# Performance work log

Measured on AMD Instinct MI355X. Metric: run time of the kernel, lower is better.

## Reference

```python
import jax, jax.numpy as jnp
import numpy as np

N, E, D_IN, D_HID, D_OUT = 50000, 600000, 128, 128, 64


def setup_inputs() -> dict:
    key = jax.random.key(0)
    ks = jax.random.split(key, 8)
    x = jax.random.normal(ks[0], (N, D_IN), dtype=jnp.float32)
    edge_index = jax.random.randint(ks[1], (2, E), 0, N, dtype=jnp.int64)
    def glorot(k, fan_in, fan_out):
        s = (6.0 / (fan_in + fan_out)) ** 0.5
        return jax.random.uniform(k, (fan_in, fan_out), jnp.float32, -s, s)
    return {
        "x": x,
        "W1": glorot(ks[2], D_IN, D_HID), "b1": jnp.zeros((D_HID,), jnp.float32),
        "W2": glorot(ks[3], D_HID, D_HID), "b2": jnp.zeros((D_HID,), jnp.float32),
        "W3": glorot(ks[4], D_HID, D_OUT), "b3": jnp.zeros((D_OUT,), jnp.float32),
        "edge_index": edge_index,
    }


def reference(x, W1, b1, W2, b2, W3, b3, edge_index):
    n = x.shape[0]
    # GCN with self-loops: A_hat = A + I, norm = D^-1/2 A_hat D^-1/2
    loops = jnp.arange(n, dtype=edge_index.dtype)
    row = jnp.concatenate([edge_index[0], loops])  # source nodes
    col = jnp.concatenate([edge_index[1], loops])  # target nodes
    deg = jax.ops.segment_sum(jnp.ones_like(col, dtype=x.dtype), col, num_segments=n)
    dinv = jnp.where(deg > 0, jax.lax.rsqrt(deg), 0.0)
    norm = dinv[row] * dinv[col]  # [E+N]

    def gcn_conv(h, W, b):
        hw = h @ W                                   # [N, out]
        msg = hw[row] * norm[:, None]                # [E+N, out] gather + scale
        return jax.ops.segment_sum(msg, col, num_segments=n) + b

    h = jax.nn.relu(gcn_conv(x, W1, b1))
    h = jax.nn.relu(gcn_conv(h, W2, b2))
    return gcn_conv(h, W3, b3)
```

## Files before the change

### kernel.cpp

```cpp
#include <hip/hip_runtime.h>
#include <hip/hip_bf16.h>
#include <hip/hip_fp16.h>


typedef _Float16 h2 __attribute__((ext_vector_type(2)));
typedef _Float16 h8 __attribute__((ext_vector_type(8)));

__device__ inline float4 h4_to_f4(float2 raw) {
    __half2 lo = *reinterpret_cast<__half2*>(&raw.x);
    __half2 hi = *reinterpret_cast<__half2*>(&raw.y);
    float2 a = __half22float2(lo);
    float2 b = __half22float2(hi);
    return make_float4(a.x, a.y, b.x, b.y);
}

__device__ inline uint pack_h2(float a, float b) {
    __half2 h = __floats2half2_rn(a, b);
    return *reinterpret_cast<uint*>(&h);
}

__global__ __launch_bounds__(256) void zero_counts_kernel(int4* __restrict__ p, int n4) {
    int i = blockIdx.x * 256 + threadIdx.x;
    if (i < n4) p[i] = make_int4(0, 0, 0, 0);
}

__global__ __launch_bounds__(256) void f32_to_f16_kernel(const float4* __restrict__ in,
                                                         uint2* __restrict__ out, int n4) {
    int i = blockIdx.x * 256 + threadIdx.x;
    if (i < n4) {
        float4 v = in[i];
        out[i] = make_uint2(pack_h2(v.x, v.y), pack_h2(v.z, v.w));
    }
}

__global__ void count_edges_kernel(const int* __restrict__ col, int* __restrict__ counts, int E) {
    int e = blockIdx.x * blockDim.x + threadIdx.x;
    if (e < E) atomicAdd(&counts[col[e]], 1);
}

__global__ __launch_bounds__(256) void block_sum_kernel(const int* __restrict__ counts,
                                                        int* __restrict__ blocksum, int n) {
    int i = blockIdx.x * 256 + threadIdx.x;
    int v = (i < n) ? counts[i] : 0;
    #pragma unroll
    for (int d = 1; d < 64; d <<= 1) v += __shfl_xor(v, d);
    __shared__ int ws[4];
    if ((threadIdx.x & 63) == 0) ws[threadIdx.x >> 6] = v;
    __syncthreads();
    if (threadIdx.x == 0) blocksum[blockIdx.x] = ws[0] + ws[1] + ws[2] + ws[3];
}

__global__ __launch_bounds__(256) void scan_sums_kernel(const int* __restrict__ blocksum,
                                                        int* __restrict__ blockoff,
                                                        int* __restrict__ offsets, int nb, int n) {
    int tid = threadIdx.x;
    int lane = tid & 63, wid = tid >> 6;
    int orig = (tid < nb) ? blocksum[tid] : 0;
    int v = orig;
    #pragma unroll
    for (int d = 1; d < 64; d <<= 1) {
        int u = __shfl_up(v, d);
        if (lane >= d) v += u;
    }
    __shared__ int ws[4];
    if (lane == 63) ws[wid] = v;
    __syncthreads();
    int add = 0;
    for (int w = 0; w < wid; ++w) add += ws[w];
    v += add;
    if (tid < nb) blockoff[tid] = v - orig;
    if (tid == 255) offsets[n] = v;
}

__global__ __launch_bounds__(256) void write_offsets_kernel(const int* __restrict__ counts,
                                                            const int* __restrict__ blockoff,
                                                            int* __restrict__ offsets,
                                                            int* __restrict__ cursor,
                                                            float* __restrict__ dinv, int n) {
    int tid = threadIdx.x;
    int i = blockIdx.x * 256 + tid;
    int lane = tid & 63, wid = tid >> 6;
    int c = (i < n) ? counts[i] : 0;
    int v = c;
    #pragma unroll
    for (int d = 1; d < 64; d <<= 1) {
        int u = __shfl_up(v, d);
        if (lane >= d) v += u;
    }
    __shared__ int ws[4];
    if (lane == 63) ws[wid] = v;
    __syncthreads();
    int add = 0;
    for (int w = 0; w < wid; ++w) add += ws[w];
    int incl = v + add;
    if (i < n) {
        offsets[i] = blockoff[blockIdx.x] + incl - c;
        cursor[i] = 0;
        dinv[i] = rsqrtf((float)(c + 1));
    }
}

__global__ void fill_csr_kernel(const int* __restrict__ row, const int* __restrict__ col,
                                const int* __restrict__ offsets, int* __restrict__ cursor,
                                const float* __restrict__ dinv,
                                int2* __restrict__ edges, int E) {
    int e = blockIdx.x * blockDim.x + threadIdx.x;
    if (e < E) {
        int c = col[e];
        int r = row[e];
        int pos = offsets[c] + atomicAdd(&cursor[c], 1);
        edges[pos] = make_int2(r, __float_as_int(dinv[r] * dinv[c]));
    }
}

template <int DO>
__global__ __launch_bounds__(256, 2) void gemm16_kernel(const __half* __restrict__ A,
                                                        const float* __restrict__ W,
                                                        __half* __restrict__ out, int n) {
    constexpr int K = 128;
    constexpr int COLTH = DO / 8;
    constexpr int ROWTH = 256 / COLTH;
    constexpr int R = (DO == 128) ? 8 : 4;
    constexpr int BR = ROWTH * R;
    constexpr int HALF = DO / 2;

    __shared__ alignas(16) h2 Wl[(K / 2) * DO];

    int tid = threadIdx.x;
    for (int idx = tid; idx < (K / 2) * (DO / 4); idx += 256) {
        int k2 = idx / (DO / 4);
        int c4 = idx % (DO / 4);
        float4 w0 = ((const float4*)(W + (size_t)(2 * k2) * DO))[c4];
        float4 w1 = ((const float4*)(W + (size_t)(2 * k2 + 1) * DO))[c4];
        h2* dst = &Wl[k2 * DO + c4 * 4];
        h2 d0; d0.x = (_Float16)w0.x; d0.y = (_Float16)w1.x; dst[0] = d0;
        h2 d1; d1.x = (_Float16)w0.y; d1.y = (_Float16)w1.y; dst[1] = d1;
        h2 d2; d2.x = (_Float16)w0.z; d2.y = (_Float16)w1.z; dst[2] = d2;
        h2 d3; d3.x = (_Float16)w0.w; d3.y = (_Float16)w1.w; dst[3] = d3;
    }
    __syncthreads();

    int ct = tid % COLTH;
    int rt = tid / COLTH;
    int rb = blockIdx.x * BR + rt * R;

    int rowc[R];
    #pragma unroll
    for (int i = 0; i < R; ++i) {
        int row = rb + i;
        rowc[i] = (row < n) ? row : (n - 1);
    }

    float acc[R][8];
    #pragma unroll
    for (int i = 0; i < R; ++i)
        #pragma unroll
        for (int c = 0; c < 8; ++c) acc[i][c] = 0.f;

    #pragma unroll 2
    for (int k8 = 0; k8 < K / 8; ++k8) {
        h8 av[R];
        #pragma unroll
        for (int i = 0; i < R; ++i) {
            av[i] = ((const h8*)(A + (size_t)rowc[i] * K))[k8];
        }
        #pragma unroll
        for (int kk = 0; kk < 4; ++kk) {
            int k2 = k8 * 4 + kk;
            h2 w0[4], w1[4];
            *(uint4*)w0 = *(const uint4*)(&Wl[k2 * DO + ct * 4]);
            *(uint4*)w1 = *(const uint4*)(&Wl[k2 * DO + HALF + ct * 4]);
            #pragma unroll
            for (int i = 0; i < R; ++i) {
                h2 a; a.x = av[i][2 * kk]; a.y = av[i][2 * kk + 1];
                #pragma unroll
                for (int c = 0; c < 4; ++c) {
                    acc[i][c]     = __builtin_amdgcn_fdot2(a, w0[c], acc[i][c], false);
                    acc[i][4 + c] = __builtin_amdgcn_fdot2(a, w1[c], acc[i][4 + c], false);
                }
            }
        }
    }

    #pragma unroll
    for (int i = 0; i < R; ++i) {
        int row = rb + i;
        if (row < n) {
            uint2 q0 = make_uint2(pack_h2(acc[i][0], acc[i][1]), pack_h2(acc[i][2], acc[i][3]));
            uint2 q1 = make_uint2(pack_h2(acc[i][4], acc[i][5]), pack_h2(acc[i][6], acc[i][7]));
            *(uint2*)(out + (size_t)row * DO + ct * 4) = q0;
            *(uint2*)(out + (size_t)row * DO + HALF + ct * 4) = q1;
        }
    }
}

template <int DO, bool RELU, bool F16OUT>
__global__ __launch_bounds__(256) void agg_kernel(const __half* __restrict__ hw,
                                                  const int* __restrict__ offsets,
                                                  const int2* __restrict__ edges,
                                                  const float* __restrict__ dinv,
                                                  const float* __restrict__ bias,
                                                  void* __restrict__ outp, int n) {
    constexpr int TPD = DO / 4;
    constexpr int DPB = 256 / TPD;
    int d = blockIdx.x * DPB + threadIdx.x / TPD;
    int j = threadIdx.x % TPD;
    if (d >= n) return;

    const float2* hw2 = (const float2*)hw;
    int beg = offsets[d];
    int end = offsets[d + 1];
    float di = dinv[d];
    float sw = di * di;

    float4 b4 = ((const float4*)bias)[j];
    float4 self = h4_to_f4(hw2[(size_t)d * TPD + j]);
    float4 acc;
    acc.x = b4.x + self.x * sw;
    acc.y = b4.y + self.y * sw;
    acc.z = b4.z + self.z * sw;
    acc.w = b4.w + self.w * sw;

    int e = beg;
    for (; e + 8 <= end; e += 8) {
        int2 r0 = edges[e + 0], r1 = edges[e + 1], r2 = edges[e + 2], r3 = edges[e + 3];
        int2 r4 = edges[e + 4], r5 = edges[e + 5], r6 = edges[e + 6], r7 = edges[e + 7];
        float4 v0 = h4_to_f4(hw2[(size_t)r0.x * TPD + j]);
        float4 v1 = h4_to_f4(hw2[(size_t)r1.x * TPD + j]);
        float4 v2 = h4_to_f4(hw2[(size_t)r2.x * TPD + j]);
        float4 v3 = h4_to_f4(hw2[(size_t)r3.x * TPD + j]);
        float4 v4 = h4_to_f4(hw2[(size_t)r4.x * TPD + j]);
        float4 v5 = h4_to_f4(hw2[(size_t)r5.x * TPD + j]);
        float4 v6 = h4_to_f4(hw2[(size_t)r6.x * TPD + j]);
        float4 v7 = h4_to_f4(hw2[(size_t)r7.x * TPD + j]);
        float w0 = __int_as_float(r0.y), w1 = __int_as_float(r1.y);
        float w2 = __int_as_float(r2.y), w3 = __int_as_float(r3.y);
        float w4 = __int_as_float(r4.y), w5 = __int_as_float(r5.y);
        float w6 = __int_as_float(r6.y), w7 = __int_as_float(r7.y);
        acc.x += v0.x * w0; acc.y += v0.y * w0; acc.z += v0.z * w0; acc.w += v0.w * w0;
        acc.x += v1.x * w1; acc.y += v1.y * w1; acc.z += v1.z * w1; acc.w += v1.w * w1;
        acc.x += v2.x * w2; acc.y += v2.y * w2; acc.z += v2.z * w2; acc.w += v2.w * w2;
        acc.x += v3.x * w3; acc.y += v3.y * w3; acc.z += v3.z * w3; acc.w += v3.w * w3;
        acc.x += v4.x * w4; acc.y += v4.y * w4; acc.z += v4.z * w4; acc.w += v4.w * w4;
        acc.x += v5.x * w5; acc.y += v5.y * w5; acc.z += v5.z * w5; acc.w += v5.w * w5;
        acc.x += v6.x * w6; acc.y += v6.y * w6; acc.z += v6.z * w6; acc.w += v6.w * w6;
        acc.x += v7.x * w7; acc.y += v7.y * w7; acc.z += v7.z * w7; acc.w += v7.w * w7;
    }
    for (; e + 4 <= end; e += 4) {
        int2 r0 = edges[e + 0], r1 = edges[e + 1], r2 = edges[e + 2], r3 = edges[e + 3];
        float4 v0 = h4_to_f4(hw2[(size_t)r0.x * TPD + j]);
        float4 v1 = h4_to_f4(hw2[(size_t)r1.x * TPD + j]);
        float4 v2 = h4_to_f4(hw2[(size_t)r2.x * TPD + j]);
        float4 v3 = h4_to_f4(hw2[(size_t)r3.x * TPD + j]);
        float w0 = __int_as_float(r0.y), w1 = __int_as_float(r1.y);
        float w2 = __int_as_float(r2.y), w3 = __int_as_float(r3.y);
        acc.x += v0.x * w0; acc.y += v0.y * w0; acc.z += v0.z * w0; acc.w += v0.w * w0;
        acc.x += v1.x * w1; acc.y += v1.y * w1; acc.z += v1.z * w1; acc.w += v1.w * w1;
        acc.x += v2.x * w2; acc.y += v2.y * w2; acc.z += v2.z * w2; acc.w += v2.w * w2;
        acc.x += v3.x * w3; acc.y += v3.y * w3; acc.z += v3.z * w3; acc.w += v3.w * w3;
    }
    for (; e < end; ++e) {
        int2 er = edges[e];
        float w = __int_as_float(er.y);
        float4 v = h4_to_f4(hw2[(size_t)er.x * TPD + j]);
        acc.x += v.x * w; acc.y += v.y * w; acc.z += v.z * w; acc.w += v.w * w;
    }

    if (RELU) {
        acc.x = fmaxf(acc.x, 0.f); acc.y = fmaxf(acc.y, 0.f);
        acc.z = fmaxf(acc.z, 0.f); acc.w = fmaxf(acc.w, 0.f);
    }
    if (F16OUT) {
        uint2 q = make_uint2(pack_h2(acc.x, acc.y), pack_h2(acc.z, acc.w));
        ((uint2*)outp)[(size_t)d * TPD + j] = q;
    } else {
        ((float4*)outp)[(size_t)d * TPD + j] = acc;
    }
}

extern "C" void kernel_launch(void* const* d_in, const int* in_sizes, int n_in,
                              void* d_out, int out_size, void* d_ws, size_t ws_size,
                              hipStream_t stream) {
    const float* x  = (const float*)d_in[0];
    const float* W1 = (const float*)d_in[1];
    const float* b1 = (const float*)d_in[2];
    const float* W2 = (const float*)d_in[3];
    const float* b2 = (const float*)d_in[4];
    const float* W3 = (const float*)d_in[5];
    const float* b3 = (const float*)d_in[6];
    const int*   ei = (const int*)d_in[7];

    const int N = in_sizes[0] / 128;
    const int E = in_sizes[7] / 2;
    const int* rowi = ei;
    const int* coli = ei + E;

    float* out = (float*)d_out;

    char* ws = (char*)d_ws;
    size_t off = 0;
    auto alloc = [&](size_t bytes) -> void* {
        void* p = ws + off;
        off = (off + bytes + 255) & ~(size_t)255;
        return p;
    };
    const int NB = (N + 255) / 256;
    float* dinv     = (float*)alloc((size_t)N * 4);
    int*   counts   = (int*)  alloc(((size_t)N + 4) * 4);
    int*   offsets  = (int*)  alloc((size_t)(N + 1) * 4);
    int*   cursor   = (int*)  alloc((size_t)N * 4);
    int*   blocksum = (int*)  alloc((size_t)NB * 4);
    int*   blockoff = (int*)  alloc((size_t)NB * 4);
    int2*  edges    = (int2*) alloc((size_t)E * 8);
    __half* x16     = (__half*)alloc((size_t)N * 128 * 2);
    __half* hw16    = (__half*)alloc((size_t)N * 128 * 2);
    __half* h16     = (__half*)alloc((size_t)N * 128 * 2);

    const int n4 = (N + 3) / 4;
    zero_counts_kernel<<<(n4 + 255) / 256, 256, 0, stream>>>((int4*)counts, n4);
    count_edges_kernel<<<(E + 255) / 256, 256, 0, stream>>>(coli, counts, E);
    block_sum_kernel<<<NB, 256, 0, stream>>>(counts, blocksum, N);
    scan_sums_kernel<<<1, 256, 0, stream>>>(blocksum, blockoff, offsets, NB, N);
    write_offsets_kernel<<<NB, 256, 0, stream>>>(counts, blockoff, offsets, cursor, dinv, N);
    fill_csr_kernel<<<(E + 255) / 256, 256, 0, stream>>>(rowi, coli, offsets, cursor, dinv, edges, E);
    const int xc4 = N * 128 / 4;
    f32_to_f16_kernel<<<(xc4 + 255) / 256, 256, 0, stream>>>((const float4*)x, (uint2*)x16, xc4);

    gemm16_kernel<128><<<(N + 127) / 128, 256, 0, stream>>>(x16, W1, hw16, N);
    agg_kernel<128, true, true><<<(N + 7) / 8, 256, 0, stream>>>(hw16, offsets, edges, dinv, b1, h16, N);

    gemm16_kernel<128><<<(N + 127) / 128, 256, 0, stream>>>(h16, W2, hw16, N);
    agg_kernel<128, true, true><<<(N + 7) / 8, 256, 0, stream>>>(hw16, offsets, edges, dinv, b2, h16, N);

    gemm16_kernel<64><<<(N + 127) / 128, 256, 0, stream>>>(h16, W3, hw16, N);
    agg_kernel<64, false, false><<<(N + 15) / 16, 256, 0, stream>>>(hw16, offsets, edges, dinv, b3, out, N);
}
```

Before: 221.0 us.

## Factor symmetric normalization into GEMM epilogue and aggregation, drop per-edge weights

Splits the D^-1/2 A D^-1/2 normalization so the GEMM epilogue scales each row by dinv[src] and aggregation scales the summed result by dinv[dst]. The CSR now stores only source indices (4 bytes per edge instead of 8), which shrinks edge traffic in fill_csr and in all three aggregation passes and removes the per-edge multiply. The trade-off is an extra dinv load and multiply per row in the GEMM epilogue, and fp16 rounding now applies to the pre-scaled values.

```diff
diff --git a/kernel.cpp b/kernel.cpp
--- a/kernel.cpp
+++ b/kernel.cpp
@@ -102,20 +102,19 @@
 
 __global__ void fill_csr_kernel(const int* __restrict__ row, const int* __restrict__ col,
                                 const int* __restrict__ offsets, int* __restrict__ cursor,
-                                const float* __restrict__ dinv,
-                                int2* __restrict__ edges, int E) {
+                                int* __restrict__ srcs, int E) {
     int e = blockIdx.x * blockDim.x + threadIdx.x;
     if (e < E) {
         int c = col[e];
-        int r = row[e];
         int pos = offsets[c] + atomicAdd(&cursor[c], 1);
-        edges[pos] = make_int2(r, __float_as_int(dinv[r] * dinv[c]));
+        srcs[pos] = row[e];
     }
 }
 
 template <int DO>
 __global__ __launch_bounds__(256, 2) void gemm16_kernel(const __half* __restrict__ A,
                                                         const float* __restrict__ W,
+                                                        const float* __restrict__ dinv,
                                                         __half* __restrict__ out, int n) {
     constexpr int K = 128;
     constexpr int COLTH = DO / 8;
@@ -186,8 +185,11 @@
     for (int i = 0; i < R; ++i) {
         int row = rb + i;
         if (row < n) {
-            uint2 q0 = make_uint2(pack_h2(acc[i][0], acc[i][1]), pack_h2(acc[i][2], acc[i][3]));
-            uint2 q1 = make_uint2(pack_h2(acc[i][4], acc[i][5]), pack_h2(acc[i][6], acc[i][7]));
+            float dv = dinv[row];
+            uint2 q0 = make_uint2(pack_h2(acc[i][0] * dv, acc[i][1] * dv),
+                                  pack_h2(acc[i][2] * dv, acc[i][3] * dv));
+            uint2 q1 = make_uint2(pack_h2(acc[i][4] * dv, acc[i][5] * dv),
+                                  pack_h2(acc[i][6] * dv, acc[i][7] * dv));
             *(uint2*)(out + (size_t)row * DO + ct * 4) = q0;
             *(uint2*)(out + (size_t)row * DO + HALF + ct * 4) = q1;
         }
@@ -197,7 +199,7 @@
 template <int DO, bool RELU, bool F16OUT>
 __global__ __launch_bounds__(256) void agg_kernel(const __half* __restrict__ hw,
                                                   const int* __restrict__ offsets,
-                                                  const int2* __restrict__ edges,
+                                                  const int* __restrict__ srcs,
                                                   const float* __restrict__ dinv,
                                                   const float* __restrict__ bias,
                                                   void* __restrict__ outp, int n) {
@@ -210,61 +212,52 @@
     const float2* hw2 = (const float2*)hw;
     int beg = offsets[d];
     int end = offsets[d + 1];
-    float di = dinv[d];
-    float sw = di * di;
-
-    float4 b4 = ((const float4*)bias)[j];
-    float4 self = h4_to_f4(hw2[(size_t)d * TPD + j]);
-    float4 acc;
-    acc.x = b4.x + self.x * sw;
-    acc.y = b4.y + self.y * sw;
-    acc.z = b4.z + self.z * sw;
-    acc.w = b4.w + self.w * sw;
+
+    float4 acc = h4_to_f4(hw2[(size_t)d * TPD + j]);
 
     int e = beg;
     for (; e + 8 <= end; e += 8) {
-        int2 r0 = edges[e + 0], r1 = edges[e + 1], r2 = edges[e + 2], r3 = edges[e + 3];
-        int2 r4 = edges[e + 4], r5 = edges[e + 5], r6 = edges[e + 6], r7 = edges[e + 7];
-        float4 v0 = h4_to_f4(hw2[(size_t)r0.x * TPD + j]);
-        float4 v1 = h4_to_f4(hw2[(size_t)r1.x * TPD + j]);
-        float4 v2 = h4_to_f4(hw2[(size_t)r2.x * TPD + j]);
-        float4 v3 = h4_to_f4(hw2[(size_t)r3.x * TPD + j]);
-        float4 v4 = h4_to_f4(hw2[(size_t)r4.x * TPD + j]);
-        float4 v5 = h4_to_f4(hw2[(size_t)r5.x * TPD + j]);
-        float4 v6 = h4_to_f4(hw2[(size_t)r6.x * TPD + j]);
-        float4 v7 = h4_to_f4(hw2[(size_t)r7.x * TPD + j]);
-        float w0 = __int_as_float(r0.y), w1 = __int_as_float(r1.y);
-        float w2 = __int_as_float(r2.y), w3 = __int_as_float(r3.y);
-        float w4 = __int_as_float(r4.y), w5 = __int_as_float(r5.y);
-        float w6 = __int_as_float(r6.y), w7 = __int_as_float(r7.y);
-        acc.x += v0.x * w0; acc.y += v0.y * w0; acc.z += v0.z * w0; acc.w += v0.w * w0;
-        acc.x += v1.x * w1; acc.y += v1.y * w1; acc.z += v1.z * w1; acc.w += v1.w * w1;
-        acc.x += v2.x * w2; acc.y += v2.y * w2; acc.z += v2.z * w2; acc.w += v2.w * w2;
-        acc.x += v3.x * w3; acc.y += v3.y * w3; acc.z += v3.z * w3; acc.w += v3.w * w3;
-        acc.x += v4.x * w4; acc.y += v4.y * w4; acc.z += v4.z * w4; acc.w += v4.w * w4;
-        acc.x += v5.x * w5; acc.y += v5.y * w5; acc.z += v5.z * w5; acc.w += v5.w * w5;
-        acc.x += v6.x * w6; acc.y += v6.y * w6; acc.z += v6.z * w6; acc.w += v6.w * w6;
-        acc.x += v7.x * w7; acc.y += v7.y * w7; acc.z += v7.z * w7; acc.w += v7.w * w7;
+        int s0 = srcs[e + 0], s1 = srcs[e + 1], s2 = srcs[e + 2], s3 = srcs[e + 3];
+        int s4 = srcs[e + 4], s5 = srcs[e + 5], s6 = srcs[e + 6], s7 = srcs[e + 7];
+        float4 v0 = h4_to_f4(hw2[(size_t)s0 * TPD + j]);
+        float4 v1 = h4_to_f4(hw2[(size_t)s1 * TPD + j]);
+        float4 v2 = h4_to_f4(hw2[(size_t)s2 * TPD + j]);
+        float4 v3 = h4_to_f4(hw2[(size_t)s3 * TPD + j]);
+        float4 v4 = h4_to_f4(hw2[(size_t)s4 * TPD + j]);
+        float4 v5 = h4_to_f4(hw2[(size_t)s5 * TPD + j]);
+        float4 v6 = h4_to_f4(hw2[(size_t)s6 * TPD + j]);
+        float4 v7 = h4_to_f4(hw2[(size_t)s7 * TPD + j]);
+        acc.x += v0.x; acc.y += v0.y; acc.z += v0.z; acc.w += v0.w;
+        acc.x += v1.x; acc.y += v1.y; acc.z += v1.z; acc.w += v1.w;
+        acc.x += v2.x; acc.y += v2.y; acc.z += v2.z; acc.w += v2.w;
+        acc.x += v3.x; acc.y += v3.y; acc.z += v3.z; acc.w += v3.w;
+        acc.x += v4.x; acc.y += v4.y; acc.z += v4.z; acc.w += v4.w;
+        acc.x += v5.x; acc.y += v5.y; acc.z += v5.z; acc.w += v5.w;
+        acc.x += v6.x; acc.y += v6.y; acc.z += v6.z; acc.w += v6.w;
+        acc.x += v7.x; acc.y += v7.y; acc.z += v7.z; acc.w += v7.w;
     }
     for (; e + 4 <= end; e += 4) {
-        int2 r0 = edges[e + 0], r1 = edges[e + 1], r2 = edges[e + 2], r3 = edges[e + 3];
-        float4 v0 = h4_to_f4(hw2[(size_t)r0.x * TPD + j]);
-        float4 v1 = h4_to_f4(hw2[(size_t)r1.x * TPD + j]);
-        float4 v2 = h4_to_f4(hw2[(size_t)r2.x * TPD + j]);
-        float4 v3 = h4_to_f4(hw2[(size_t)r3.x * TPD + j]);
-        float w0 = __int_as_float(r0.y), w1 = __int_as_float(r1.y);
-        float w2 = __int_as_float(r2.y), w3 = __int_as_float(r3.y);
-        acc.x += v0.x * w0; acc.y += v0.y * w0; acc.z += v0.z * w0; acc.w += v0.w * w0;
-        acc.x += v1.x * w1; acc.y += v1.y * w1; acc.z += v1.z * w1; acc.w += v1.w * w1;
-        acc.x += v2.x * w2; acc.y += v2.y * w2; acc.z += v2.z * w2; acc.w += v2.w * w2;
-        acc.x += v3.x * w3; acc.y += v3.y * w3; acc.z += v3.z * w3; acc.w += v3.w * w3;
+        int s0 = srcs[e + 0], s1 = srcs[e + 1], s2 = srcs[e + 2], s3 = srcs[e + 3];
+        float4 v0 = h4_to_f4(hw2[(size_t)s0 * TPD + j]);
+        float4 v1 = h4_to_f4(hw2[(size_t)s1 * TPD + j]);
+        float4 v2 = h4_to_f4(hw2[(size_t)s2 * TPD + j]);
+        float4 v3 = h4_to_f4(hw2[(size_t)s3 * TPD + j]);
+        acc.x += v0.x; acc.y += v0.y; acc.z += v0.z; acc.w += v0.w;
+        acc.x += v1.x; acc.y += v1.y; acc.z += v1.z; acc.w += v1.w;
+        acc.x += v2.x; acc.y += v2.y; acc.z += v2.z; acc.w += v2.w;
+        acc.x += v3.x; acc.y += v3.y; acc.z += v3.z; acc.w += v3.w;
     }
     for (; e < end; ++e) {
-        int2 er = edges[e];
-        float w = __int_as_float(er.y);
-        float4 v = h4_to_f4(hw2[(size_t)er.x * TPD + j]);
-        acc.x += v.x * w; acc.y += v.y * w; acc.z += v.z * w; acc.w += v.w * w;
-    }
+        float4 v = h4_to_f4(hw2[(size_t)srcs[e] * TPD + j]);
+        acc.x += v.x; acc.y += v.y; acc.z += v.z; acc.w += v.w;
+    }
+
+    float di = dinv[d];
+    float4 b4 = ((const float4*)bias)[j];
+    acc.x = b4.x + di * acc.x;
+    acc.y = b4.y + di * acc.y;
+    acc.z = b4.z + di * acc.z;
+    acc.w = b4.w + di * acc.w;
 
     if (RELU) {
         acc.x = fmaxf(acc.x, 0.f); acc.y = fmaxf(acc.y, 0.f);
@@ -311,7 +304,7 @@
     int*   cursor   = (int*)  alloc((size_t)N * 4);
     int*   blocksum = (int*)  alloc((size_t)NB * 4);
     int*   blockoff = (int*)  alloc((size_t)NB * 4);
-    int2*  edges    = (int2*) alloc((size_t)E * 8);
+    int*   srcs     = (int*)  alloc((size_t)E * 4);
     __half* x16     = (__half*)alloc((size_t)N * 128 * 2);
     __half* hw16    = (__half*)alloc((size_t)N * 128 * 2);
     __half* h16     = (__half*)alloc((size_t)N * 128 * 2);
@@ -322,16 +315,16 @@
     block_sum_kernel<<<NB, 256, 0, stream>>>(counts, blocksum, N);
     scan_sums_kernel<<<1, 256, 0, stream>>>(blocksum, blockoff, offsets, NB, N);
     write_offsets_kernel<<<NB, 256, 0, stream>>>(counts, blockoff, offsets, cursor, dinv, N);
-    fill_csr_kernel<<<(E + 255) / 256, 256, 0, stream>>>(rowi, coli, offsets, cursor, dinv, edges, E);
+    fill_csr_kernel<<<(E + 255) / 256, 256, 0, stream>>>(rowi, coli, offsets, cursor, srcs, E);
     const int xc4 = N * 128 / 4;
     f32_to_f16_kernel<<<(xc4 + 255) / 256, 256, 0, stream>>>((const float4*)x, (uint2*)x16, xc4);
 
-    gemm16_kernel<128><<<(N + 127) / 128, 256, 0, stream>>>(x16, W1, hw16, N);
-    agg_kernel<128, true, true><<<(N + 7) / 8, 256, 0, stream>>>(hw16, offsets, edges, dinv, b1, h16, N);
-
-    gemm16_kernel<128><<<(N + 127) / 128, 256, 0, stream>>>(h16, W2, hw16, N);
-    agg_kernel<128, true, true><<<(N + 7) / 8, 256, 0, stream>>>(hw16, offsets, edges, dinv, b2, h16, N);
-
-    gemm16_kernel<64><<<(N + 127) / 128, 256, 0, stream>>>(h16, W3, hw16, N);
-    agg_kernel<64, false, false><<<(N + 15) / 16, 256, 0, stream>>>(hw16, offsets, edges, dinv, b3, out, N);
-}
+    gemm16_kernel<128><<<(N + 127) / 128, 256, 0, stream>>>(x16, W1, dinv, hw16, N);
+    agg_kernel<128, true, true><<<(N + 7) / 8, 256, 0, stream>>>(hw16, offsets, srcs, dinv, b1, h16, N);
+
+    gemm16_kernel<128><<<(N + 127) / 128, 256, 0, stream>>>(h16, W2, dinv, hw16, N);
+    agg_kernel<128, true, true><<<(N + 7) / 8, 256, 0, stream>>>(hw16, offsets, srcs, dinv, b2, h16, N);
+
+    gemm16_kernel<64><<<(N + 127) / 128, 256, 0, stream>>>(h16, W3, dinv, hw16, N);
+    agg_kernel<64, false, false><<<(N + 15) / 16, 256, 0, stream>>>(hw16, offsets, srcs, dinv, b3, out, N);
+}
```

Result: no change. 223.5 us (+1.1%).
